# Kernel optimization log

Measured on AMD Instinct MI355X. Metric: run time of the kernel, lower is better.

The kernel has to match this reference:

```python
import jax, jax.numpy as jnp
import numpy as np

S, B, L = 64, 32, 64          # seq_len (messages), batch (convs), max tokens per message
V, D = 32000, 300             # vocab, embedding dim
H = 512                       # hidden_dim; per-direction message hidden = H//2
F = 16                        # num_game_features
Hh = H // 2


def lstm_dir(x, mask, Wih, Whh, b, reverse=False):
    """Masked (packed-equivalent) LSTM. x:(T,N,D), mask:(T,N) bool.
    Returns h:(T,N,H) with zeros at invalid steps (matches pad_packed_sequence)."""
    if reverse:
        x, mask = x[::-1], mask[::-1]
    N = x.shape[1]
    Hd = Whh.shape[1]
    xg = jnp.einsum('tnd,gd->tng', x, Wih) + b  # (T,N,4H) input gates precomputed

    def step(carry, inp):
        h, c = carry
        xg_t, m = inp
        g = xg_t + h @ Whh.T
        i, f, gg, o = jnp.split(g, 4, axis=-1)
        c_new = jax.nn.sigmoid(f) * c + jax.nn.sigmoid(i) * jnp.tanh(gg)
        h_new = jax.nn.sigmoid(o) * jnp.tanh(c_new)
        m = m[:, None]
        return (jnp.where(m, h_new, h), jnp.where(m, c_new, c)), jnp.where(m, h_new, 0.0)

    init = (jnp.zeros((N, Hd), x.dtype), jnp.zeros((N, Hd), x.dtype))
    _, hs = jax.lax.scan(step, init, (xg, mask))
    if reverse:
        hs = hs[::-1]
    return hs


def setup_inputs() -> dict:
    key = jax.random.key(0)
    ks = jax.random.split(key, 16)
    s = 1.0 / np.sqrt(Hh)
    sc = 1.0 / np.sqrt(H)
    inp = {
        'messages': jax.random.randint(ks[0], (S, B, L), 0, V),
        'game_features': jax.random.normal(ks[1], (S, B, F), jnp.float32),
        'conv_lengths': jax.random.randint(ks[2], (B,), 1, S + 1),
        'E': jax.random.normal(ks[3], (V, D), jnp.float32) * 0.1,  # frozen embedding
        # message bi-LSTM (forward dir)
        'Wih_f': jax.random.uniform(ks[4], (4 * Hh, D), jnp.float32, -s, s),
        'Whh_f': jax.random.uniform(ks[5], (4 * Hh, Hh), jnp.float32, -s, s),
        'b_f': jax.random.uniform(ks[6], (4 * Hh,), jnp.float32, -s, s),
        # message bi-LSTM (backward dir)
        'Wih_b': jax.random.uniform(ks[7], (4 * Hh, D), jnp.float32, -s, s),
        'Whh_b': jax.random.uniform(ks[8], (4 * Hh, Hh), jnp.float32, -s, s),
        'b_b': jax.random.uniform(ks[9], (4 * Hh,), jnp.float32, -s, s),
        # conversation LSTM
        'Wih_c': jax.random.uniform(ks[10], (4 * H, H), jnp.float32, -sc, sc),
        'Whh_c': jax.random.uniform(ks[11], (4 * H, H), jnp.float32, -sc, sc),
        'b_c': jax.random.uniform(ks[12], (4 * H,), jnp.float32, -sc, sc),
        # classifier
        'Wc': jax.random.uniform(ks[13], (H + F,), jnp.float32, -sc, sc),
        'bc': jax.random.uniform(ks[14], (), jnp.float32, -sc, sc),
    }
    return inp


def reference(messages, game_features, conv_lengths, E, Wih_f, Whh_f, b_f,
              Wih_b, Whh_b, b_b, Wih_c, Whh_c, b_c, Wc, bc):
    # ---- message level: all S*B messages in one batched bi-LSTM pass ----
    flat = messages.reshape(S * B, L)                       # (N, L)
    emb = E[flat]                                           # (N, L, D)
    msg_len = jnp.maximum((flat != 0).sum(1), 1)            # clamp(min=1)
    tmask = jnp.arange(L)[:, None] < msg_len[None, :]       # (L, N)
    x = emb.transpose(1, 0, 2)                              # (L, N, D) time-major
    h_fwd = lstm_dir(x, tmask, Wih_f, Whh_f, b_f, reverse=False)
    h_bwd = lstm_dir(x, tmask, Wih_b, Whh_b, b_b, reverse=True)
    h = jnp.concatenate([h_fwd, h_bwd], axis=-1)            # (L, N, H); zeros at pad
    enc = h.max(axis=0)                                     # maxpool incl. zero pads (torch semantics)
    enc = enc.reshape(S, B, H)
    # ---- conversation level ----
    cmask = jnp.arange(S)[:, None] < conv_lengths[None, :]  # (S, B)
    conv_out = lstm_dir(enc, cmask, Wih_c, Whh_c, b_c)      # (S, B, H), zeros past length
    # dropout is identity at inference
    combined = jnp.concatenate([conv_out, game_features], axis=2)  # (S, B, H+F)
    logits = combined @ Wc + bc                             # (S, B)
    return logits
```

## Files before the change

### kernel.cpp

```cpp
#include <hip/hip_runtime.h>
#include <cmath>

#define S_DIM 64
#define B_DIM 32
#define L_DIM 64
#define NMSG  2048
#define D_DIM 300
#define HH    256
#define HC    512
#define F_DIM 16
#define VOCAB 32000

#define OFF_XGV   0u
#define OFF_WHH   32768000u
#define OFF_WPI   33030144u
#define OFF_WCI   33357824u
#define OFF_WCR   33882112u
#define OFF_ENCB  34406400u
#define OFF_HCONV 34930688u
#define OFF_CCONV 34938880u
#define OFF_CO    34955264u
#define OFF_MLEN  36003840u

typedef __attribute__((ext_vector_type(8))) short s8v;
typedef __attribute__((ext_vector_type(4))) float f4v;
#define MFMA(a,b,c) __builtin_amdgcn_mfma_f32_16x16x32_bf16((a),(b),(c),0,0,0)

__device__ __forceinline__ unsigned short f2bf(float x) {
    unsigned u = __float_as_uint(x);
    return (unsigned short)((u + 0x7FFFu + ((u >> 16) & 1u)) >> 16);
}
__device__ __forceinline__ float bf2f(unsigned short u) {
    return __uint_as_float(((unsigned)u) << 16);
}
__device__ __forceinline__ float sigm(float x) { return 1.0f / (1.0f + __expf(-x)); }
__device__ __forceinline__ float tanh_f(float x) { return 1.0f - 2.0f / (1.0f + __expf(2.0f * x)); }

__device__ __forceinline__ void gload16(const unsigned short* g, unsigned short* l) {
    __builtin_amdgcn_global_load_lds(
        (const __attribute__((address_space(1))) unsigned int*)g,
        (__attribute__((address_space(3))) unsigned int*)l, 16, 0, 0);
}

__global__ __launch_bounds__(256) void pack_whh(
    const float* __restrict__ Whh_f, const float* __restrict__ Whh_b,
    unsigned short* __restrict__ Wp)
{
    int wv = blockIdx.x >> 3, kt = blockIdx.x & 7, dir = blockIdx.y;
    const float* W = dir ? Whh_b : Whh_f;
    int tid = threadIdx.x, lane = tid & 63, g = tid >> 6;
    int n = (g * 16 + wv) * 16 + (lane & 15);
    int k0 = kt * 32 + (lane >> 4) * 8;
    unsigned short tmp[8];
    #pragma unroll
    for (int u = 0; u < 8; ++u) tmp[u] = f2bf(W[(size_t)n * HH + k0 + u]);
    *(uint4*)(Wp + (((size_t)(dir * 16 + wv) * 8 + kt) * 4 + g) * 512 + lane * 8) = *(uint4*)tmp;
}

__global__ __launch_bounds__(256) void pack_wih(
    const float* __restrict__ Wih_f, const float* __restrict__ Wih_b,
    unsigned short* __restrict__ wpi)
{
    int nt = blockIdx.x, dir = blockIdx.y;
    const float* W = dir ? Wih_b : Wih_f;
    int tid = threadIdx.x, lane = tid & 63, ktq = tid >> 6;
    int n = nt * 16 + (lane & 15);
    int kb = (lane >> 4) * 8;
    for (int kt = ktq; kt < 10; kt += 4) {
        int k0 = kt * 32 + kb;
        unsigned short tmp[8];
        #pragma unroll
        for (int u = 0; u < 8; ++u) {
            int k = k0 + u;
            tmp[u] = (k < D_DIM) ? f2bf(W[(size_t)n * D_DIM + k]) : (unsigned short)0;
        }
        *(uint4*)(wpi + (size_t)dir * 327680 + ((size_t)(nt * 10 + kt)) * 512 + lane * 8) = *(uint4*)tmp;
    }
}

__global__ __launch_bounds__(256) void pack_whc(
    const float* __restrict__ Wih_c, const float* __restrict__ Whh_c,
    unsigned short* __restrict__ whci, unsigned short* __restrict__ whcr)
{
    int nt = blockIdx.x, which = blockIdx.y;
    const float* W = which ? Whh_c : Wih_c;
    unsigned short* dst = which ? whcr : whci;
    int tid = threadIdx.x, lane = tid & 63;
    int row = nt * 16 + (lane & 15);
    int kb = (lane >> 4) * 8;
    for (int kt = tid >> 6; kt < 16; kt += 4) {
        int k0 = kt * 32 + kb;
        unsigned short tmp[8];
        #pragma unroll
        for (int u = 0; u < 8; ++u) tmp[u] = f2bf(W[(size_t)row * HC + k0 + u]);
        *(uint4*)(dst + ((size_t)(nt * 16 + kt)) * 512 + lane * 8) = *(uint4*)tmp;
    }
}

__global__ __launch_bounds__(256) void msg_len_kernel(const int* __restrict__ msgs,
                                                      int* __restrict__ mlen) {
    int n = blockIdx.x * 256 + threadIdx.x;
    if (n >= NMSG) return;
    int cnt = 0;
    #pragma unroll 8
    for (int l = 0; l < L_DIM; ++l) cnt += (msgs[n * L_DIM + l] != 0);
    mlen[n] = max(cnt, 1);
}

__global__ __launch_bounds__(256) void init_conv(float* __restrict__ ws) {
    unsigned i = blockIdx.x * 256u + threadIdx.x;
    if (i < 24576u) ws[OFF_HCONV + i] = 0.0f;
}

#define EROW 328
__global__ __launch_bounds__(256) void xg_gemm(
    const float* __restrict__ E,
    const float* __restrict__ b_f, const float* __restrict__ b_b,
    const unsigned short* __restrict__ wpi,
    unsigned short* __restrict__ xgv)
{
    __shared__ __align__(16) unsigned short e_lds[32 * EROW];
    const int w0 = blockIdx.x * 32;
    const int dirb = blockIdx.y;
    const float* bias = dirb ? b_b : b_f;

    const int tid = threadIdx.x, lane = tid & 63, wv = tid >> 6;
    const int l15 = lane & 15, kg = lane >> 4;

    {
        const float4* E4 = (const float4*)(E + (size_t)w0 * D_DIM);
        for (int i = tid; i < 32 * 75; i += 256) {
            int r = i / 75, c = i - r * 75;
            float4 v = E4[r * 75 + c];
            unsigned short t4[4] = { f2bf(v.x), f2bf(v.y), f2bf(v.z), f2bf(v.w) };
            *(uint2*)&e_lds[r * EROW + c * 4] = *(uint2*)t4;
        }
        for (int i = tid; i < 32 * 20; i += 256) {
            int r = i / 20, c = i - r * 20;
            e_lds[r * EROW + 300 + c] = 0;
        }
    }
    __syncthreads();

    s8v a0q[10], a1q[10];
    #pragma unroll
    for (int kt = 0; kt < 10; ++kt) {
        a0q[kt] = *(const s8v*)&e_lds[l15 * EROW + kt * 32 + kg * 8];
        a1q[kt] = *(const s8v*)&e_lds[(16 + l15) * EROW + kt * 32 + kg * 8];
    }

    const unsigned short* wb = wpi + (size_t)dirb * 327680;
    const f4v zf = {0.0f, 0.0f, 0.0f, 0.0f};

    #pragma unroll
    for (int jt = 0; jt < 4; ++jt) {
        f4v acc[2][4];
        #pragma unroll
        for (int m = 0; m < 2; ++m)
            #pragma unroll
            for (int g = 0; g < 4; ++g) acc[m][g] = zf;

        #pragma unroll
        for (int kt = 0; kt < 10; ++kt) {
            #pragma unroll
            for (int g = 0; g < 4; ++g) {
                int nt = g * 16 + jt * 4 + wv;
                s8v b = *(const s8v*)(wb + ((size_t)(nt * 10 + kt)) * 512 + lane * 8);
                acc[0][g] = MFMA(a0q[kt], b, acc[0][g]);
                acc[1][g] = MFMA(a1q[kt], b, acc[1][g]);
            }
        }

        const int j = jt * 64 + wv * 16 + l15;
        float bv[4];
        #pragma unroll
        for (int g = 0; g < 4; ++g) bv[g] = bias[g * 256 + j];
        const int colp = (jt * 2 + (wv >> 1)) * 128 + l15 * 8 + (wv & 1) * 4;
        #pragma unroll
        for (int m = 0; m < 2; ++m)
            #pragma unroll
            for (int r = 0; r < 4; ++r) {
                int w = w0 + m * 16 + kg * 4 + r;
                unsigned short t4[4];
                #pragma unroll
                for (int g = 0; g < 4; ++g) t4[g] = f2bf(acc[m][g][r] + bv[g]);
                *(uint2*)(xgv + ((size_t)dirb * VOCAB + w) * 1024 + colp) = *(uint2*)t4;
            }
    }
}

#define XGS  1032
#define HROW 264
__global__ __launch_bounds__(1024, 1) void word_lstm(
    const int* __restrict__ msgs, const int* __restrict__ mlen,
    const unsigned short* __restrict__ xgv,
    const unsigned short* __restrict__ whh,
    unsigned short* __restrict__ enc_bf)
{
    __shared__ __align__(16) unsigned short xg_lds[2][16 * XGS];
    __shared__ __align__(16) unsigned short h_lds[2][16 * HROW];
    __shared__ int tok_s[16 * 64];
    __shared__ int len_s[16];

    const int mg = blockIdx.x >> 1, dir = blockIdx.x & 1;
    const int tid = threadIdx.x, lane = tid & 63, wv = tid >> 6;
    const int l15 = lane & 15, kg = lane >> 4;

    for (int i = tid; i < 16 * 64; i += 1024) tok_s[i] = msgs[mg * 1024 + i];
    if (tid < 16) len_s[tid] = mlen[mg * 16 + tid];
    for (int i = tid; i < 2 * 16 * HROW; i += 1024) h_lds[0][i] = 0;
    __syncthreads();

    const unsigned short* xv = xgv + (size_t)dir * VOCAB * 1024;

    const unsigned short* wbase = whh + (size_t)(dir * 16 + wv) * 16384 + lane * 8;
    const unsigned short* bp[8];
    #pragma unroll
    for (int kt = 0; kt < 8; ++kt) bp[kt] = wbase + kt * 2048;

    int lens[4];
    #pragma unroll
    for (int r = 0; r < 4; ++r) lens[r] = len_s[kg * 4 + r];

    int bmax = 1;
    #pragma unroll
    for (int i = 0; i < 16; ++i) bmax = max(bmax, len_s[i]);

    float c_st[4], rm[4];
    unsigned short hbf[4];
    #pragma unroll
    for (int r = 0; r < 4; ++r) { c_st[r] = 0.0f; rm[r] = -INFINITY; hbf[r] = 0; }

    const int qoff = (wv >> 1) * 128 + l15 * 8 + (wv & 1) * 4;

    {
        int tt = dir ? (len_s[wv] - 1) : 0;
        if (tt < 0) tt = 0;
        const unsigned short* src = xv + (size_t)tok_s[wv * 64 + tt] * 1024 + lane * 8;
        gload16(src,       &xg_lds[0][wv * XGS]);
        gload16(src + 512, &xg_lds[0][wv * XGS + 512]);
    }

    for (int t = 0; t < bmax; ++t) {
        __syncthreads();
        const int buf = t & 1;
        const int hbuf = t & 1;

        if (t + 1 < bmax) {
            int tn = t + 1;
            int tt = dir ? (len_s[wv] - 1 - tn) : tn;
            if (tt < 0) tt = 0;
            const unsigned short* src = xv + (size_t)tok_s[wv * 64 + tt] * 1024 + lane * 8;
            gload16(src,       &xg_lds[buf ^ 1][wv * XGS]);
            gload16(src + 512, &xg_lds[buf ^ 1][wv * XGS + 512]);
        }

        f4v acc[4];
        {
            uint2 q[4];
            #pragma unroll
            for (int r = 0; r < 4; ++r)
                q[r] = *(const uint2*)&xg_lds[buf][(kg * 4 + r) * XGS + qoff];
            #pragma unroll
            for (int g = 0; g < 4; ++g) {
                f4v v;
                #pragma unroll
                for (int r = 0; r < 4; ++r) {
                    unsigned w = (g & 2) ? q[r].y : q[r].x;
                    v[r] = (g & 1) ? __uint_as_float(w & 0xFFFF0000u)
                                   : __uint_as_float(w << 16);
                }
                acc[g] = v;
            }
        }

        #pragma unroll
        for (int kt = 0; kt < 8; ++kt) {
            s8v a = *(const s8v*)&h_lds[hbuf][l15 * HROW + kt * 32 + kg * 8];
            const unsigned short* pw = bp[kt];
            acc[0] = MFMA(a, *(const s8v*)(pw),        acc[0]);
            acc[1] = MFMA(a, *(const s8v*)(pw + 512),  acc[1]);
            acc[2] = MFMA(a, *(const s8v*)(pw + 1024), acc[2]);
            acc[3] = MFMA(a, *(const s8v*)(pw + 1536), acc[3]);
        }

        #pragma unroll
        for (int r = 0; r < 4; ++r) {
            float gi = acc[0][r], gf = acc[1][r], gc = acc[2][r], go = acc[3][r];
            float cn = sigm(gf) * c_st[r] + sigm(gi) * tanh_f(gc);
            float hn = sigm(go) * tanh_f(cn);
            if (t < lens[r]) {
                c_st[r] = cn;
                rm[r] = fmaxf(rm[r], hn);
                hbf[r] = f2bf(hn);
            }
            h_lds[hbuf ^ 1][(kg * 4 + r) * HROW + wv * 16 + l15] = hbf[r];
        }
    }

    #pragma unroll
    for (int r = 0; r < 4; ++r) {
        float v = rm[r];
        if (lens[r] < 64) v = fmaxf(v, 0.0f);
        enc_bf[(size_t)(mg * 16 + kg * 4 + r) * HC + dir * HH + wv * 16 + l15] = f2bf(v);
    }
}

#define CROW 520
__global__ __launch_bounds__(256) void xgc_gemm(
    const unsigned short* __restrict__ enc_bf,
    const unsigned short* __restrict__ whci,
    const float* __restrict__ b_c,
    unsigned short* __restrict__ xgc)
{
    __shared__ __align__(16) unsigned short e_lds[32 * CROW];
    const int m0 = blockIdx.x * 32;
    const int n0 = blockIdx.y * 256;
    const int tid = threadIdx.x, lane = tid & 63, wv = tid >> 6;
    const int l15 = lane & 15, kg = lane >> 4;

    for (int i = tid; i < 2048; i += 256) {
        int row = i >> 6, u4 = i & 63;
        ((uint4*)&e_lds[row * CROW])[u4] = ((const uint4*)(enc_bf + (size_t)(m0 + row) * HC))[u4];
    }
    __syncthreads();

    const f4v zf = {0.0f, 0.0f, 0.0f, 0.0f};
    f4v acc[2][4];
    #pragma unroll
    for (int m = 0; m < 2; ++m)
        #pragma unroll
        for (int q = 0; q < 4; ++q) acc[m][q] = zf;

    for (int kt = 0; kt < 16; ++kt) {
        s8v a0 = *(const s8v*)&e_lds[l15 * CROW + kt * 32 + kg * 8];
        s8v a1 = *(const s8v*)&e_lds[(16 + l15) * CROW + kt * 32 + kg * 8];
        #pragma unroll
        for (int q = 0; q < 4; ++q) {
            int nt = (n0 >> 4) + wv * 4 + q;
            s8v b = *(const s8v*)(whci + ((size_t)(nt * 16 + kt)) * 512 + lane * 8);
            acc[0][q] = MFMA(a0, b, acc[0][q]);
            acc[1][q] = MFMA(a1, b, acc[1][q]);
        }
    }

    #pragma unroll
    for (int q = 0; q < 4; ++q) {
        int col = n0 + (wv * 4 + q) * 16 + l15;
        float bv = b_c[col];
        #pragma unroll
        for (int m = 0; m < 2; ++m)
            #pragma unroll
            for (int r = 0; r < 4; ++r)
                xgc[(size_t)(m0 + m * 16 + kg * 4 + r) * 2048 + col] = f2bf(acc[m][q][r] + bv);
    }
}

__global__ __launch_bounds__(256) void conv_step(
    const unsigned short* __restrict__ whcr,
    const unsigned short* __restrict__ xgc,
    const int* __restrict__ conv_len,
    unsigned short* __restrict__ h_bf,
    float* __restrict__ c_ws,
    float* __restrict__ co,
    int s)
{
    __shared__ __align__(16) unsigned short xh[32 * CROW];
    __shared__ float gbuf[4][32][16];

    const int tid = threadIdx.x, jb = blockIdx.x;
    const int lane = tid & 63, g = tid >> 6;
    const int l15 = lane & 15, kg = lane >> 4;

    for (int i = tid; i < 2048; i += 256) {
        int row = i >> 6, u4 = i & 63;
        ((uint4*)&xh[row * CROW])[u4] = ((const uint4*)(h_bf + (size_t)row * HC))[u4];
    }
    __syncthreads();

    const int col = g * 512 + jb * 16 + l15;
    f4v acc0, acc1;
    #pragma unroll
    for (int r = 0; r < 4; ++r) {
        acc0[r] = bf2f(xgc[(size_t)(s * B_DIM + kg * 4 + r) * 2048 + col]);
        acc1[r] = bf2f(xgc[(size_t)(s * B_DIM + 16 + kg * 4 + r) * 2048 + col]);
    }

    const int nt = g * 32 + jb;
    for (int kt = 0; kt < 16; ++kt) {
        s8v a0 = *(const s8v*)&xh[l15 * CROW + kt * 32 + kg * 8];
        s8v a1 = *(const s8v*)&xh[(16 + l15) * CROW + kt * 32 + kg * 8];
        s8v b  = *(const s8v*)(whcr + ((size_t)(nt * 16 + kt)) * 512 + lane * 8);
        acc0 = MFMA(a0, b, acc0);
        acc1 = MFMA(a1, b, acc1);
    }

    #pragma unroll
    for (int r = 0; r < 4; ++r) {
        gbuf[g][kg * 4 + r][l15]      = acc0[r];
        gbuf[g][16 + kg * 4 + r][l15] = acc1[r];
    }
    __syncthreads();

    #pragma unroll
    for (int u = 0; u < 2; ++u) {
        int cell = tid + 256 * u;
        int b = cell >> 4, jj = cell & 15;
        int j = jb * 16 + jj;
        bool valid = s < conv_len[b];
        float g_i = gbuf[0][b][jj], g_f = gbuf[1][b][jj];
        float g_c = gbuf[2][b][jj], g_o = gbuf[3][b][jj];
        float cold = c_ws[b * HC + j];
        float cn = sigm(g_f) * cold + sigm(g_i) * tanh_f(g_c);
        float hn = sigm(g_o) * tanh_f(cn);
        float outv = 0.0f;
        if (valid) {
            c_ws[b * HC + j] = cn;
            h_bf[b * HC + j] = f2bf(hn);
            outv = hn;
        }
        co[((size_t)s * B_DIM + b) * HC + j] = outv;
    }
}

__global__ __launch_bounds__(256) void logits_kernel(
    const float* __restrict__ gfeat, const float* __restrict__ Wc, const float* __restrict__ bc,
    const float* __restrict__ co, float* __restrict__ out)
{
    int o = blockIdx.x * 4 + (threadIdx.x >> 6);
    int lane = threadIdx.x & 63;
    const float* row = co + (size_t)o * HC;
    float sum = 0.0f;
    #pragma unroll
    for (int u = 0; u < 8; ++u) sum += row[lane + 64 * u] * Wc[lane + 64 * u];
    if (lane < F_DIM) sum += gfeat[o * F_DIM + lane] * Wc[HC + lane];
    #pragma unroll
    for (int off = 32; off > 0; off >>= 1) sum += __shfl_down(sum, off, 64);
    if (lane == 0) out[o] = sum + bc[0];
}

extern "C" void kernel_launch(void* const* d_in, const int* in_sizes, int n_in,
                              void* d_out, int out_size, void* d_ws, size_t ws_size,
                              hipStream_t stream) {
    const int*   msgs    = (const int*)  d_in[0];
    const float* gfeat   = (const float*)d_in[1];
    const int*   convlen = (const int*)  d_in[2];
    const float* E       = (const float*)d_in[3];
    const float* Wih_f   = (const float*)d_in[4];
    const float* Whh_f   = (const float*)d_in[5];
    const float* b_f     = (const float*)d_in[6];
    const float* Wih_b   = (const float*)d_in[7];
    const float* Whh_b   = (const float*)d_in[8];
    const float* b_b     = (const float*)d_in[9];
    const float* Wih_c   = (const float*)d_in[10];
    const float* Whh_c   = (const float*)d_in[11];
    const float* b_c     = (const float*)d_in[12];
    const float* Wc      = (const float*)d_in[13];
    const float* bc      = (const float*)d_in[14];
    float* out = (float*)d_out;
    float* ws  = (float*)d_ws;

    unsigned short* xgv    = (unsigned short*)(ws + OFF_XGV);
    unsigned short* xgc    = (unsigned short*)(ws + OFF_XGV);
    unsigned short* whh    = (unsigned short*)(ws + OFF_WHH);
    unsigned short* wpi    = (unsigned short*)(ws + OFF_WPI);
    unsigned short* whci   = (unsigned short*)(ws + OFF_WCI);
    unsigned short* whcr   = (unsigned short*)(ws + OFF_WCR);
    unsigned short* enc_bf = (unsigned short*)(ws + OFF_ENCB);
    unsigned short* h_bf   = (unsigned short*)(ws + OFF_HCONV);
    float*          c_ws   = ws + OFF_CCONV;
    float*          co     = ws + OFF_CO;
    int*            mlen   = (int*)(ws + OFF_MLEN);

    pack_whh<<<dim3(128, 2), 256, 0, stream>>>(Whh_f, Whh_b, whh);
    pack_wih<<<dim3(64, 2), 256, 0, stream>>>(Wih_f, Wih_b, wpi);
    pack_whc<<<dim3(128, 2), 256, 0, stream>>>(Wih_c, Whh_c, whci, whcr);
    msg_len_kernel<<<NMSG / 256, 256, 0, stream>>>(msgs, mlen);
    init_conv<<<96, 256, 0, stream>>>(ws);
    xg_gemm<<<dim3(1000, 2), 256, 0, stream>>>(E, b_f, b_b, wpi, xgv);

    word_lstm<<<256, 1024, 0, stream>>>(msgs, mlen, xgv, whh, enc_bf);

    xgc_gemm<<<dim3(64, 8), 256, 0, stream>>>(enc_bf, whci, b_c, xgc);

    for (int s = 0; s < S_DIM; ++s)
        conv_step<<<32, 256, 0, stream>>>(whcr, xgc, convlen, h_bf, c_ws, co, s);

    logits_kernel<<<NMSG / 4, 256, 0, stream>>>(gfeat, Wc, bc, co, out);
}
```

Measured before the change: 1.157 ms.

## Fuse logits projection into conv_step via atomics and remap word_lstm block order

The final logits projection now happens inside each conv_step. Each step reduces h*Wc across 16 lanes and atomically adds the partial sum into the output, which a new small kernel pre-initialises with the game-feature term and bias. This removes the full conv_out buffer write and the separate logits kernel pass. The word_lstm block index mapping is also permuted so that forward and backward directions of neighbouring message groups are scheduled differently, likely to improve cache locality or load balance. Float atomics make the summation order nondeterministic.

```diff
diff --git a/kernel.cpp b/kernel.cpp
--- a/kernel.cpp
+++ b/kernel.cpp
@@ -112,6 +112,18 @@
     if (i < 24576u) ws[OFF_HCONV + i] = 0.0f;
 }
 
+__global__ __launch_bounds__(256) void logits_init(
+    const float* __restrict__ gfeat, const float* __restrict__ Wc, const float* __restrict__ bc,
+    float* __restrict__ out)
+{
+    int o = blockIdx.x * 256 + threadIdx.x;
+    if (o >= NMSG) return;
+    float s = bc[0];
+    #pragma unroll
+    for (int f = 0; f < F_DIM; ++f) s += gfeat[o * F_DIM + f] * Wc[HC + f];
+    out[o] = s;
+}
+
 #define EROW 328
 __global__ __launch_bounds__(256) void xg_gemm(
     const float* __restrict__ E,
@@ -202,7 +214,9 @@
     __shared__ int tok_s[16 * 64];
     __shared__ int len_s[16];
 
-    const int mg = blockIdx.x >> 1, dir = blockIdx.x & 1;
+    const int bid = blockIdx.x;
+    const int dir = (bid >> 2) & 1;
+    const int mg  = (bid & 3) | ((bid >> 3) << 2);
     const int tid = threadIdx.x, lane = tid & 63, wv = tid >> 6;
     const int l15 = lane & 15, kg = lane >> 4;
 
@@ -362,7 +376,8 @@
     const int* __restrict__ conv_len,
     unsigned short* __restrict__ h_bf,
     float* __restrict__ c_ws,
-    float* __restrict__ co,
+    const float* __restrict__ Wc,
+    float* __restrict__ out,
     int s)
 {
     __shared__ __align__(16) unsigned short xh[32 * CROW];
@@ -402,41 +417,29 @@
     }
     __syncthreads();
 
+    const int bA = tid >> 4, jj = tid & 15;
+    const int j = jb * 16 + jj;
+    const float wcj = Wc[j];
     #pragma unroll
     for (int u = 0; u < 2; ++u) {
-        int cell = tid + 256 * u;
-        int b = cell >> 4, jj = cell & 15;
-        int j = jb * 16 + jj;
+        int b = bA + 16 * u;
         bool valid = s < conv_len[b];
         float g_i = gbuf[0][b][jj], g_f = gbuf[1][b][jj];
         float g_c = gbuf[2][b][jj], g_o = gbuf[3][b][jj];
         float cold = c_ws[b * HC + j];
         float cn = sigm(g_f) * cold + sigm(g_i) * tanh_f(g_c);
         float hn = sigm(g_o) * tanh_f(cn);
-        float outv = 0.0f;
+        float hval = 0.0f;
         if (valid) {
             c_ws[b * HC + j] = cn;
             h_bf[b * HC + j] = f2bf(hn);
-            outv = hn;
-        }
-        co[((size_t)s * B_DIM + b) * HC + j] = outv;
-    }
-}
-
-__global__ __launch_bounds__(256) void logits_kernel(
-    const float* __restrict__ gfeat, const float* __restrict__ Wc, const float* __restrict__ bc,
-    const float* __restrict__ co, float* __restrict__ out)
-{
-    int o = blockIdx.x * 4 + (threadIdx.x >> 6);
-    int lane = threadIdx.x & 63;
-    const float* row = co + (size_t)o * HC;
-    float sum = 0.0f;
-    #pragma unroll
-    for (int u = 0; u < 8; ++u) sum += row[lane + 64 * u] * Wc[lane + 64 * u];
-    if (lane < F_DIM) sum += gfeat[o * F_DIM + lane] * Wc[HC + lane];
-    #pragma unroll
-    for (int off = 32; off > 0; off >>= 1) sum += __shfl_down(sum, off, 64);
-    if (lane == 0) out[o] = sum + bc[0];
+            hval = hn;
+        }
+        float p = hval * wcj;
+        #pragma unroll
+        for (int off = 8; off; off >>= 1) p += __shfl_down(p, off, 16);
+        if (jj == 0 && p != 0.0f) atomicAdd(&out[s * B_DIM + b], p);
+    }
 }
 
 extern "C" void kernel_launch(void* const* d_in, const int* in_sizes, int n_in,
@@ -469,7 +472,6 @@
     unsigned short* enc_bf = (unsigned short*)(ws + OFF_ENCB);
     unsigned short* h_bf   = (unsigned short*)(ws + OFF_HCONV);
     float*          c_ws   = ws + OFF_CCONV;
-    float*          co     = ws + OFF_CO;
     int*            mlen   = (int*)(ws + OFF_MLEN);
 
     pack_whh<<<dim3(128, 2), 256, 0, stream>>>(Whh_f, Whh_b, whh);
@@ -477,6 +479,7 @@
     pack_whc<<<dim3(128, 2), 256, 0, stream>>>(Wih_c, Whh_c, whci, whcr);
     msg_len_kernel<<<NMSG / 256, 256, 0, stream>>>(msgs, mlen);
     init_conv<<<96, 256, 0, stream>>>(ws);
+    logits_init<<<NMSG / 256, 256, 0, stream>>>(gfeat, Wc, bc, out);
     xg_gemm<<<dim3(1000, 2), 256, 0, stream>>>(E, b_f, b_b, wpi, xgv);
 
     word_lstm<<<256, 1024, 0, stream>>>(msgs, mlen, xgv, whh, enc_bf);
@@ -484,7 +487,5 @@
     xgc_gemm<<<dim3(64, 8), 256, 0, stream>>>(enc_bf, whci, b_c, xgc);
 
     for (int s = 0; s < S_DIM; ++s)
-        conv_step<<<32, 256, 0, stream>>>(whcr, xgc, convlen, h_bf, c_ws, co, s);
-
-    logits_kernel<<<NMSG / 4, 256, 0, stream>>>(gfeat, Wc, bc, co, out);
-}
+        conv_step<<<32, 256, 0, stream>>>(whcr, xgc, convlen, h_bf, c_ws, Wc, out, s);
+}
```

Measured after the change: 1.262 ms. 9.1% more time.
